# Kernel tuning notes

Measured on AMD Instinct MI355X. Metric: run time of the kernel, lower is better.

## Reference

```python
import jax, jax.numpy as jnp
import numpy as np

GROUP_SIZE = 64
OUT_F, IN_F = 11008, 4096
W_SHAPE = (OUT_F, IN_F)


def quantize_q40(w):
    # w: fp32 weight, numel divisible by GROUP_SIZE
    wg = w.reshape(-1, GROUP_SIZE)                      # [N, G]
    wmax = jnp.max(jnp.abs(wg), axis=1)
    scale = (wmax / 7.0).astype(jnp.float16)[:, None]   # [N, 1] fp16 per-group scale
    quant = wg / scale.astype(jnp.float32)
    q = jnp.round(quant).astype(jnp.int8)               # values in [-7, 7]
    pairs = q.reshape(-1, 2, GROUP_SIZE)                # even rows -> MSB nibble, odd -> LSB
    packed = ((pairs[:, 0] << 4) | (pairs[:, 1] & 15)).astype(jnp.int8)  # [N/2, G]
    return packed, scale


def dequantize_q40(w, scale):
    # w: int8 packed [N/2, G]; arithmetic shifts sign-extend each nibble
    msb = w >> 4
    lsb = (w << 4) >> 4
    full = jnp.concatenate([msb, lsb], axis=1).reshape(-1, GROUP_SIZE)  # interleave back to [N, G]
    return (full.astype(jnp.float16) * scale).reshape(W_SHAPE)


def setup_inputs() -> dict:
    key = jax.random.key(0)
    kx, kw = jax.random.split(key)
    x = jax.random.normal(kx, (4, 2048, IN_F), dtype=jnp.float16)
    w_fp = jax.random.normal(kw, W_SHAPE, dtype=jnp.float32) * 0.02
    linear_w, linear_s = quantize_q40(w_fp)
    return {"x": x, "linear_w": linear_w, "linear_s": linear_s}


def reference(x, linear_w, linear_s):
    # dequantize packed int4 weights to fp16, then dense linear (no bias)
    deq = dequantize_q40(linear_w, linear_s)            # [OUT_F, IN_F] fp16
    return jnp.einsum('bsi,oi->bso', x, deq)            # F.linear(x, deq)
```

## Files before the change

### kernel.cpp

```cpp
#include <hip/hip_runtime.h>
#include <stdint.h>

#define IN_F   4096
#define OUT_F  11008
#define M_ROWS 8192
#define BM 256
#define BN 256
#define BK 64
#define NTILE_K (IN_F / BK)

typedef __attribute__((ext_vector_type(4))) float  f32x4;
typedef __attribute__((ext_vector_type(4))) int    int4v;
typedef __attribute__((ext_vector_type(4))) unsigned int uint4v;
typedef __attribute__((ext_vector_type(8))) unsigned short ushort8;
typedef _Float16 f16x8 __attribute__((ext_vector_type(8)));
typedef _Float16 f16x2 __attribute__((ext_vector_type(2)));

__global__ __launch_bounds__(256) void pack_w(const int* __restrict__ w,
                                              unsigned int* __restrict__ wq) {
  const int totald = OUT_F * (IN_F / 8);
  for (int d = blockIdx.x * blockDim.x + threadIdx.x; d < totald;
       d += gridDim.x * blockDim.x) {
    const int o   = d >> 9;
    const int k0  = (d & 511) * 8;
    const int n   = o * 64 + (k0 >> 6);
    const int p   = n >> 1;
    const int nib = n & 1;
    const int j0  = k0 & 63;
    const int* src = w + p * 64 + j0;
    const int4v b0 = __builtin_nontemporal_load(reinterpret_cast<const int4v*>(src));
    const int4v b1 = __builtin_nontemporal_load(reinterpret_cast<const int4v*>(src + 4));
    unsigned int acc = 0;
#pragma unroll
    for (int i = 0; i < 8; ++i) {
      const int b = (i < 4) ? b0[i] : b1[i - 4];
      const int q = nib ? ((b << 28) >> 28) : (b >> 4);
      acc |= ((unsigned int)((q + 8) & 0xF)) << (4 * i);
    }
    wq[d] = acc;
  }
}

__global__ __launch_bounds__(256) void scale_t(const float* __restrict__ s,
                                               unsigned short* __restrict__ st) {
  const int o = blockIdx.x * 256 + threadIdx.x;
  const int g = blockIdx.y;
  if (o < OUT_F) {
    _Float16 h = (_Float16)s[o * 64 + g];
    st[g * OUT_F + o] = __builtin_bit_cast(unsigned short, h);
  }
}

__global__ __launch_bounds__(256) void cvt_x(const float* __restrict__ x,
                                             unsigned short* __restrict__ xb) {
  const int total8 = (M_ROWS * IN_F) / 8;
  for (int t = blockIdx.x * blockDim.x + threadIdx.x; t < total8;
       t += gridDim.x * blockDim.x) {
    const f32x4 a0 = __builtin_nontemporal_load(reinterpret_cast<const f32x4*>(x + t * 8));
    const f32x4 a1 = __builtin_nontemporal_load(reinterpret_cast<const f32x4*>(x + t * 8 + 4));
    ushort8 r;
#pragma unroll
    for (int e = 0; e < 4; ++e) {
      r[e]     = __builtin_bit_cast(unsigned short, (_Float16)a0[e]);
      r[4 + e] = __builtin_bit_cast(unsigned short, (_Float16)a1[e]);
    }
    *reinterpret_cast<ushort8*>(xb + t * 8) = r;
  }
}

__device__ __forceinline__ void gld16(const void* g, void* l) {
  __builtin_amdgcn_global_load_lds(
      (const __attribute__((address_space(1))) unsigned int*)(uintptr_t)g,
      (__attribute__((address_space(3))) unsigned int*)(unsigned int)(uintptr_t)l,
      16, 0, 0);
}

#define BAR() do { asm volatile("" ::: "memory"); __builtin_amdgcn_s_barrier(); \
                   asm volatile("" ::: "memory"); } while (0)

__global__ __launch_bounds__(512, 2) void gemm_bt(const unsigned short* __restrict__ A,
                                                  const unsigned char* __restrict__ WQ,
                                                  const unsigned short* __restrict__ ST,
                                                  float* __restrict__ C) {
  __shared__ __align__(16) unsigned short lds[57344];

  const int NT  = OUT_F / BN;
  const int nwg = (M_ROWS / BM) * NT;
  const int cpx = nwg >> 3;
  const int bid = blockIdx.x;
  const int swz = (bid & 7) * cpx + (bid >> 3);
  const int mt  = swz / NT;
  const int nt  = swz - mt * NT;
  const int n0  = nt * BN;

  const int tid  = threadIdx.x;
  const int lane = tid & 63;
  const int wid  = tid >> 6;
  const int wr   = wid >> 2;
  const int wc   = wid & 3;

  const int r_st = tid >> 2;
  const int lc   = (tid & 3) ^ ((tid >> 3) & 3);
  const unsigned short* gA = A + (size_t)(mt * BM + r_st) * IN_F + lc * 8;
  unsigned short* ldsw = lds + tid * 8;

#define STAGE_A(b, h, kk) do {                                              \
    unsigned short* d_ = ldsw + (b) * 16384 + (h) * 8192;                   \
    const unsigned short* s_ = gA + (kk) + (h) * 32;                        \
    gld16(s_, d_); gld16(s_ + (size_t)128 * IN_F, d_ + 4096);               \
  } while (0)

  const unsigned char* gBQ = WQ + (size_t)(n0 + (tid >> 1)) * (IN_F / 2) + (tid & 1) * 16;
#define STAGE_BQ(b, tk) \
    gld16(gBQ + (size_t)(tk) * 32, lds + 32768 + (b) * 4096 + tid * 8)

#define STAGE_SL(c) do {                                                    \
    const int sl_ = (c) * 512 + tid;                                        \
    gld16(ST + (size_t)(sl_ >> 5) * OUT_F + n0 + (sl_ & 31) * 8,            \
          lds + 40960 + sl_ * 8);                                           \
  } while (0)

  const int fr   = lane & 15;
  const int kq   = lane >> 4;
  const int coff = (kq ^ ((fr >> 1) & 3)) * 8;

  f16x8 afr[4], bfr[4];
#define RD_A(b, h, mq) do {                                                 \
    const unsigned short* p_ = lds + (b) * 16384 + (h) * 8192 + coff;       \
    _Pragma("unroll") for (int mm = 0; mm < 4; ++mm)                        \
      afr[mm] = *reinterpret_cast<const f16x8*>(                            \
          p_ + (size_t)(wr * 128 + (mq) * 64 + mm * 16 + fr) * 32);         \
  } while (0)

#define DEQ_B(bbuf, kh, g) do {                                             \
    _Pragma("unroll") for (int nn = 0; nn < 4; ++nn) {                      \
      const int o_ = wc * 64 + nn * 16 + fr;                                \
      const unsigned int w4 = *reinterpret_cast<const unsigned int*>(       \
          lds + 32768 + (bbuf) * 4096 + o_ * 16 + (kh) * 8 + kq * 2);       \
      const _Float16 s_  = *reinterpret_cast<const _Float16*>(              \
          lds + 40960 + (g) * 256 + o_);                                    \
      const _Float16 c1_ = s_ * (_Float16)(-1024.0f);            \
      const _Float16 c8_ = s_ * (_Float16)(-8.0f);               \
      f16x2 s2; s2[0] = s_;  s2[1] = s_;                                    \
      f16x2 c1; c1[0] = c1_; c1[1] = c1_;                                   \
      f16x2 c8; c8[0] = c8_; c8[1] = c8_;                                   \
      uint4v rr;                                                            \
      _Pragma("unroll") for (int j = 0; j < 4; ++j) {                       \
        const unsigned int t_ = w4 >> (8 * j);                              \
        const unsigned int m_ = (t_ & 0xFu) | ((t_ << 12) & 0xF0000u)       \
                              | 0x64006400u;                                \
        f16x2 v_ = __builtin_bit_cast(f16x2, m_);                           \
        v_ = __builtin_elementwise_fma(v_, s2, c1);       \
        v_ = v_ + c8;                                            \
        rr[j] = __builtin_bit_cast(unsigned int, v_);                       \
      }                                                                     \
      bfr[nn] = __builtin_bit_cast(f16x8, rr);                              \
    }                                                                       \
  } while (0)

  f32x4 acc[8][4] = {};
#define MFMA16(mq) do {                                                     \
    __builtin_amdgcn_s_setprio(1);                                          \
    _Pragma("unroll") for (int mm = 0; mm < 4; ++mm)                        \
      _Pragma("unroll") for (int nn = 0; nn < 4; ++nn)                      \
        acc[(mq)*4+mm][nn] = __builtin_amdgcn_mfma_f32_16x16x32_f16(        \
            afr[mm], bfr[nn], acc[(mq)*4+mm][nn], 0, 0, 0);                 \
    __builtin_amdgcn_s_setprio(0);                                          \
  } while (0)

#define VW(n) asm volatile("s_waitcnt vmcnt(" #n ")" ::: "memory")

  STAGE_SL(0); STAGE_SL(1); STAGE_SL(2); STAGE_SL(3);
  STAGE_A(0, 0, 0);
  STAGE_BQ(0, 0);
  STAGE_A(0, 1, 0);
  STAGE_A(1, 0, BK);
  VW(4);
  BAR();

  for (int it = 0; it < NTILE_K / 2; ++it) {
    const int ta  = 2 * it;
    const int tb  = 2 * it + 1;
    const int tna = (2 * it + 2) & (NTILE_K - 1);
    const int tnb = (2 * it + 3) & (NTILE_K - 1);

    STAGE_A(1, 1, tb * BK);
    DEQ_B(0, 0, ta); RD_A(0, 0, 0);
    BAR(); MFMA16(0);
    STAGE_BQ(1, tb);
    RD_A(0, 0, 1);
    VW(5);
    BAR(); MFMA16(1);
    STAGE_A(0, 0, tna * BK);
    DEQ_B(0, 1, ta); RD_A(0, 1, 0);
    BAR(); MFMA16(0);
    STAGE_BQ(0, tna);
    RD_A(0, 1, 1);
    VW(3);
    BAR(); MFMA16(1);
    STAGE_A(0, 1, tna * BK);
    DEQ_B(1, 0, tb); RD_A(1, 0, 0);
    BAR(); MFMA16(0);
    RD_A(1, 0, 1);
    BAR(); MFMA16(1);
    STAGE_A(1, 0, tnb * BK);
    DEQ_B(1, 1, tb); RD_A(1, 1, 0);
    BAR(); MFMA16(0);
    RD_A(1, 1, 1);
    VW(4);
    BAR(); MFMA16(1);
  }

  asm volatile("s_waitcnt vmcnt(0)" ::: "memory");

  const int col  = n0 + wc * 64 + fr;
  const int row0 = mt * BM + wr * 128 + (lane >> 4) * 4;
#pragma unroll
  for (int m = 0; m < 8; ++m) {
#pragma unroll
    for (int n = 0; n < 4; ++n) {
      float* cp = C + (size_t)(row0 + m * 16) * OUT_F + (col + n * 16);
#pragma unroll
      for (int r = 0; r < 4; ++r) cp[(size_t)r * OUT_F] = acc[m][n][r];
    }
  }
}

extern "C" void kernel_launch(void* const* d_in, const int* in_sizes, int n_in,
                              void* d_out, int out_size, void* d_ws, size_t ws_size,
                              hipStream_t stream) {
  const float* x = (const float*)d_in[0];
  const int*   w = (const int*)d_in[1];
  const float* s = (const float*)d_in[2];
  float*     out = (float*)d_out;

  unsigned short* xb = (unsigned short*)d_ws;
  unsigned char*  wq = (unsigned char*)d_ws + (size_t)M_ROWS * IN_F * 2;
  unsigned short* st = (unsigned short*)(wq + (size_t)OUT_F * (IN_F / 2));

  pack_w<<<dim3(2048), dim3(256), 0, stream>>>(w, (unsigned int*)wq);
  scale_t<<<dim3(43, 64), dim3(256), 0, stream>>>(s, st);
  cvt_x<<<dim3(2048), dim3(256), 0, stream>>>(x, xb);
  gemm_bt<<<dim3((M_ROWS / BM) * (OUT_F / BN)), dim3(512), 0, stream>>>(xb, wq, st, out);
}
```

Before: 855.6 us.

## Double-buffer MFMA fragments, swizzle packed-weight LDS layout, simplify nibble dequant

Adds separate A and B register fragment sets so the LDS reads and dequantization for the next MFMA block are issued before the current MFMA block, which software-pipelines LDS latency behind matrix math. It also XOR-swizzles the packed 4-bit weight tile in LDS to cut bank conflicts. The nibble order is permuted during packing so each f16x2 pair is pulled out with a single shift and mask. The cost is higher register pressure from the extra fragments, plus retuned waitcnt and barrier placement that has to keep buffer reuse race-free.

```diff
diff --git a/kernel.cpp b/kernel.cpp
--- a/kernel.cpp
+++ b/kernel.cpp
@@ -35,7 +35,8 @@
     for (int i = 0; i < 8; ++i) {
       const int b = (i < 4) ? b0[i] : b1[i - 4];
       const int q = nib ? ((b << 28) >> 28) : (b >> 4);
-      acc |= ((unsigned int)((q + 8) & 0xF)) << (4 * i);
+      const int pos = (i >> 1) + ((i & 1) << 2);
+      acc |= ((unsigned int)((q + 8) & 0xF)) << (4 * pos);
     }
     wq[d] = acc;
   }
@@ -110,7 +111,8 @@
     gld16(s_, d_); gld16(s_ + (size_t)128 * IN_F, d_ + 4096);               \
   } while (0)
 
-  const unsigned char* gBQ = WQ + (size_t)(n0 + (tid >> 1)) * (IN_F / 2) + (tid & 1) * 16;
+  const int bql = tid ^ ((tid >> 3) & 7);
+  const unsigned char* gBQ = WQ + (size_t)(n0 + (bql >> 1)) * (IN_F / 2) + (bql & 1) * 16;
 #define STAGE_BQ(b, tk) \
     gld16(gBQ + (size_t)(tk) * 32, lds + 32768 + (b) * 4096 + tid * 8)
 
@@ -124,19 +126,21 @@
   const int kq   = lane >> 4;
   const int coff = (kq ^ ((fr >> 1) & 3)) * 8;
 
-  f16x8 afr[4], bfr[4];
-#define RD_A(b, h, mq) do {                                                 \
+  f16x8 afrA[4], afrB[4], bfrA[4], bfrB[4];
+#define RD_A(dst, b, h, mq) do {                                            \
     const unsigned short* p_ = lds + (b) * 16384 + (h) * 8192 + coff;       \
     _Pragma("unroll") for (int mm = 0; mm < 4; ++mm)                        \
-      afr[mm] = *reinterpret_cast<const f16x8*>(                            \
+      dst[mm] = *reinterpret_cast<const f16x8*>(                            \
           p_ + (size_t)(wr * 128 + (mq) * 64 + mm * 16 + fr) * 32);         \
   } while (0)
 
-#define DEQ_B(bbuf, kh, g) do {                                             \
+#define DEQ_B(dst, bbuf, kh, g) do {                                        \
     _Pragma("unroll") for (int nn = 0; nn < 4; ++nn) {                      \
       const int o_ = wc * 64 + nn * 16 + fr;                                \
+      const int s4_ = o_ * 8 + (kh) * 4 + kq;                               \
+      const int ph_ = s4_ ^ (((s4_ >> 5) & 7) << 2);                        \
       const unsigned int w4 = *reinterpret_cast<const unsigned int*>(       \
-          lds + 32768 + (bbuf) * 4096 + o_ * 16 + (kh) * 8 + kq * 2);       \
+          lds + 32768 + (bbuf) * 4096 + ph_ * 2);                           \
       const _Float16 s_  = *reinterpret_cast<const _Float16*>(              \
           lds + 40960 + (g) * 256 + o_);                                    \
       const _Float16 c1_ = s_ * (_Float16)(-1024.0f);            \
@@ -145,26 +149,25 @@
       f16x2 c1; c1[0] = c1_; c1[1] = c1_;                                   \
       f16x2 c8; c8[0] = c8_; c8[1] = c8_;                                   \
       uint4v rr;                                                            \
-      _Pragma("unroll") for (int j = 0; j < 4; ++j) {                       \
-        const unsigned int t_ = w4 >> (8 * j);                              \
-        const unsigned int m_ = (t_ & 0xFu) | ((t_ << 12) & 0xF0000u)       \
+      _Pragma("unroll") for (int p = 0; p < 4; ++p) {                       \
+        const unsigned int m_ = ((w4 >> (4 * p)) & 0x000F000Fu)             \
                               | 0x64006400u;                                \
         f16x2 v_ = __builtin_bit_cast(f16x2, m_);                           \
-        v_ = __builtin_elementwise_fma(v_, s2, c1);       \
-        v_ = v_ + c8;                                            \
-        rr[j] = __builtin_bit_cast(unsigned int, v_);                       \
+        v_ = __builtin_elementwise_fma(v_, s2, c1);                         \
+        v_ = v_ + c8;                                                       \
+        rr[p] = __builtin_bit_cast(unsigned int, v_);                       \
       }                                                                     \
-      bfr[nn] = __builtin_bit_cast(f16x8, rr);                              \
+      dst[nn] = __builtin_bit_cast(f16x8, rr);                              \
     }                                                                       \
   } while (0)
 
   f32x4 acc[8][4] = {};
-#define MFMA16(mq) do {                                                     \
+#define MFMA16(mq, aset, bset) do {                                         \
     __builtin_amdgcn_s_setprio(1);                                          \
     _Pragma("unroll") for (int mm = 0; mm < 4; ++mm)                        \
       _Pragma("unroll") for (int nn = 0; nn < 4; ++nn)                      \
         acc[(mq)*4+mm][nn] = __builtin_amdgcn_mfma_f32_16x16x32_f16(        \
-            afr[mm], bfr[nn], acc[(mq)*4+mm][nn], 0, 0, 0);                 \
+            aset[mm], bset[nn], acc[(mq)*4+mm][nn], 0, 0, 0);               \
     __builtin_amdgcn_s_setprio(0);                                          \
   } while (0)
 
@@ -177,6 +180,8 @@
   STAGE_A(1, 0, BK);
   VW(4);
   BAR();
+  RD_A(afrA, 0, 0, 0);
+  DEQ_B(bfrA, 0, 0, 0);
 
   for (int it = 0; it < NTILE_K / 2; ++it) {
     const int ta  = 2 * it;
@@ -184,31 +189,30 @@
     const int tna = (2 * it + 2) & (NTILE_K - 1);
     const int tnb = (2 * it + 3) & (NTILE_K - 1);
 
-    STAGE_A(1, 1, tb * BK);
-    DEQ_B(0, 0, ta); RD_A(0, 0, 0);
-    BAR(); MFMA16(0);
-    STAGE_BQ(1, tb);
-    RD_A(0, 0, 1);
+    STAGE_A(1, 1, tb * BK); STAGE_BQ(1, tb);
+    RD_A(afrB, 0, 0, 1);
     VW(5);
-    BAR(); MFMA16(1);
+    BAR(); MFMA16(0, afrA, bfrA);
+    RD_A(afrA, 0, 1, 0); DEQ_B(bfrB, 0, 1, ta);
+    BAR(); MFMA16(1, afrB, bfrA);
     STAGE_A(0, 0, tna * BK);
-    DEQ_B(0, 1, ta); RD_A(0, 1, 0);
-    BAR(); MFMA16(0);
+    RD_A(afrB, 0, 1, 1);
+    VW(2);
+    BAR(); MFMA16(0, afrA, bfrB);
     STAGE_BQ(0, tna);
-    RD_A(0, 1, 1);
-    VW(3);
-    BAR(); MFMA16(1);
+    RD_A(afrA, 1, 0, 0); DEQ_B(bfrA, 1, 0, tb);
+    BAR(); MFMA16(1, afrB, bfrB);
     STAGE_A(0, 1, tna * BK);
-    DEQ_B(1, 0, tb); RD_A(1, 0, 0);
-    BAR(); MFMA16(0);
-    RD_A(1, 0, 1);
-    BAR(); MFMA16(1);
+    RD_A(afrB, 1, 0, 1);
+    BAR(); MFMA16(0, afrA, bfrA);
+    RD_A(afrA, 1, 1, 0); DEQ_B(bfrB, 1, 1, tb);
+    BAR(); MFMA16(1, afrB, bfrA);
     STAGE_A(1, 0, tnb * BK);
-    DEQ_B(1, 1, tb); RD_A(1, 1, 0);
-    BAR(); MFMA16(0);
-    RD_A(1, 1, 1);
+    RD_A(afrB, 1, 1, 1);
     VW(4);
-    BAR(); MFMA16(1);
+    BAR(); MFMA16(0, afrA, bfrB);
+    RD_A(afrA, 0, 0, 0); DEQ_B(bfrA, 0, 0, tna);
+    BAR(); MFMA16(1, afrB, bfrB);
   }
 
   asm volatile("s_waitcnt vmcnt(0)" ::: "memory");
```

New measurement: 792.1 us. -7.4%, faster.
